# Kernel optimization log

Measured on AMD Instinct MI355X. Metric: run time of the kernel, lower is better.

Reference implementation:

```python
import jax, jax.numpy as jnp
import numpy as np
import math

NUM_EMBED = 1024
EMBED_FEATS = 256
IN_FEATS = 512
COMMITMENT_COST = 0.25
B, T = 16, 4096


def setup_inputs() -> dict:
    key = jax.random.key(0)
    k1, k2, k3, k4 = jax.random.split(key, 4)
    inputs = jax.random.normal(k1, (B, IN_FEATS, T), dtype=jnp.float32)
    # Conv1d(kernel_size=1) == per-position linear: weight [E, C_in], bias [E]
    proj_w = jax.random.normal(k2, (EMBED_FEATS, IN_FEATS), dtype=jnp.float32) / np.sqrt(IN_FEATS)
    proj_b = jax.random.normal(k3, (EMBED_FEATS,), dtype=jnp.float32) * 0.01
    embed = jax.random.normal(k4, (NUM_EMBED, EMBED_FEATS), dtype=jnp.float32)
    return {"inputs": inputs, "proj_w": proj_w, "proj_b": proj_b, "embed": embed}


def reference(inputs, proj_w, proj_b, embed):
    sg = jax.lax.stop_gradient
    b, c_in, t = inputs.shape
    # 1x1 conv projection then transpose(1,-1): [B, T, E]
    x = jnp.einsum('bct,ec->bte', inputs, proj_w) + proj_b
    flat = x.reshape(-1, EMBED_FEATS)  # [B*T, E]
    d2 = (jnp.sum(flat * flat, axis=1, keepdims=True)
          + jnp.sum(embed * embed, axis=1)
          - 2.0 * flat @ embed.T)  # [B*T, num_embed]
    q_idx = jnp.argmin(d2, axis=1)  # [B*T]
    # one-hot @ embed == direct gather (same math, same gradient structure)
    z_q = embed[q_idx].reshape(x.shape)  # [B, T, E]
    vq_loss = jnp.mean((z_q - sg(x)) ** 2)
    commitment_loss = jnp.mean((sg(z_q) - x) ** 2)
    loss = vq_loss + COMMITMENT_COST * commitment_loss
    z_q_st = x + sg(z_q - x)  # straight-through
    n_tokens = flat.shape[0]
    probs = jnp.zeros((NUM_EMBED,), dtype=jnp.float32).at[q_idx].add(1.0) / n_tokens
    log_perplexity = -jnp.sum(probs * jnp.log(probs + 1e-10))
    num_spatial = n_tokens / b
    kldiv_r = math.log(NUM_EMBED) * num_spatial * jnp.ones((b, 1), dtype=jnp.float32)
    z_q_out = jnp.swapaxes(z_q_st, 1, 2)  # [B, E, T]
    return z_q_out, loss, kldiv_r, log_perplexity
```

## Files before the change

### kernel.cpp

```cpp
#include <hip/hip_runtime.h>
#include <hip/hip_bf16.h>
#include <math.h>

#define TT   4096
#define BB   16
#define NTOK 65536
#define CIN  512
#define EF   256
#define NE   1024

typedef __attribute__((ext_vector_type(8))) short bf16x8;
typedef __attribute__((ext_vector_type(4))) float f32x4;

static __device__ __forceinline__ unsigned short f2bf(float f) {
  unsigned int u = __float_as_uint(f);
  u += 0x7fffu + ((u >> 16) & 1u);
  return (unsigned short)(u >> 16);
}

#define GLL(gsrc, ldst) \
  __builtin_amdgcn_global_load_lds((const __attribute__((address_space(1))) void*)(gsrc), \
                                   (__attribute__((address_space(3))) void*)(ldst), 16, 0, 0)

__global__ __launch_bounds__(256) void k_prep(const float* __restrict__ Wf,
                                              const float* __restrict__ Ef,
                                              unsigned short* __restrict__ Wbf,
                                              unsigned short* __restrict__ Ebf,
                                              float* __restrict__ e_norm) {
  int bid = blockIdx.x;
  if (bid < 512) {
    int i = bid * 256 + threadIdx.x;
    Wbf[i] = f2bf(Wf[i]);
  } else if (bid < 1536) {
    int i = (bid - 512) * 256 + threadIdx.x;
    Ebf[i] = f2bf(-2.0f * Ef[i]);
  } else {
    int w = threadIdx.x >> 6, l = threadIdx.x & 63;
    int k = (bid - 1536) * 4 + w;
    const float4 v4 = ((const float4*)(Ef + (size_t)k * EF))[l];
    float s = v4.x * v4.x + v4.y * v4.y + v4.z * v4.z + v4.w * v4.w;
    for (int off = 32; off; off >>= 1) s += __shfl_down(s, off);
    if (l == 0) e_norm[k] = s;
  }
}

__global__ __launch_bounds__(512, 2) void k_fused(const float* __restrict__ in,
                                                  const unsigned short* __restrict__ Wbf,
                                                  const float* __restrict__ bias,
                                                  const unsigned short* __restrict__ Ebf,
                                                  const float* __restrict__ e_norm,
                                                  int* __restrict__ bi_out,
                                                  unsigned int* __restrict__ hist,
                                                  float* __restrict__ sse) {
  __shared__ unsigned short lds[32768];
  unsigned short* as_ = lds;
  unsigned short* bs  = lds + 8192;
  unsigned short* xs  = lds;

  int tid = threadIdx.x;
  int w = tid >> 6, l = tid & 63;
  int l15 = l & 15, quad = l >> 4;
  int tq = w & 1, eq = w >> 1;
  int cg = w & 3, th = w >> 2;
  int tok0 = blockIdx.x * 128;
  const float* src = in + (size_t)(tok0 >> 12) * CIN * TT + (tok0 & 4095);

  f32x4 acc[4][4];
#pragma unroll
  for (int a = 0; a < 4; ++a)
#pragma unroll
    for (int b = 0; b < 4; ++b) acc[a][b] = (f32x4){0.f, 0.f, 0.f, 0.f};

  float v[16];
  {
    const float* s0 = src + (size_t)(cg * 16) * TT + th * 64 + l;
#pragma unroll
    for (int i = 0; i < 16; ++i) v[i] = s0[(size_t)i * TT];
  }
  for (int ks = 0; ks < 8; ++ks) {
    int k0 = ks * 64;
#pragma unroll
    for (int i = 0; i < 4; ++i) {
      int g = i * 512 + tid;
      int row = g >> 3, pc = g & 7, lc = pc ^ (row & 7);
      GLL(Wbf + (size_t)row * CIN + k0 + lc * 8, bs + g * 8);
    }
    int trow = th * 64 + l;
#pragma unroll
    for (int cc = 0; cc < 2; ++cc) {
      alignas(16) unsigned short tmp[8];
#pragma unroll
      for (int j = 0; j < 8; ++j) tmp[j] = f2bf(v[cc * 8 + j]);
      int c8 = cg * 2 + cc;
      int pc = c8 ^ (trow & 7);
      *(bf16x8*)(as_ + trow * 64 + pc * 8) = *(const bf16x8*)tmp;
    }
    __syncthreads();
    if (ks < 7) {
      const float* s0 = src + (size_t)(k0 + 64 + cg * 16) * TT + th * 64 + l;
#pragma unroll
      for (int i = 0; i < 16; ++i) v[i] = s0[(size_t)i * TT];
    }
#pragma unroll
    for (int kstep = 0; kstep < 2; ++kstep) {
      int ck = kstep * 4 + quad;
      bf16x8 af[4], bfr[4];
#pragma unroll
      for (int msub = 0; msub < 4; ++msub) {
        int row = tq * 64 + msub * 16 + l15;
        int pa = ck ^ (row & 7);
        af[msub] = *(const bf16x8*)(as_ + row * 64 + pa * 8);
      }
#pragma unroll
      for (int nsub = 0; nsub < 4; ++nsub) {
        int row = eq * 64 + nsub * 16 + l15;
        int pb = ck ^ (row & 7);
        bfr[nsub] = *(const bf16x8*)(bs + row * 64 + pb * 8);
      }
#pragma unroll
      for (int msub = 0; msub < 4; ++msub)
#pragma unroll
        for (int nsub = 0; nsub < 4; ++nsub)
          acc[msub][nsub] = __builtin_amdgcn_mfma_f32_16x16x32_bf16(af[msub], bfr[nsub],
                                                                    acc[msub][nsub], 0, 0, 0);
    }
    __syncthreads();
  }

  float xsq = 0.f;
#pragma unroll
  for (int nsub = 0; nsub < 4; ++nsub) {
    int e = eq * 64 + nsub * 16 + l15;
    float bv = bias[e];
    int cx = e >> 3;
#pragma unroll
    for (int msub = 0; msub < 4; ++msub)
#pragma unroll
      for (int reg = 0; reg < 4; ++reg) {
        int m = tq * 64 + msub * 16 + quad * 4 + reg;
        float x = acc[msub][nsub][reg] + bv;
        xsq += x * x;
        int pcx = cx ^ (m & 31);
        xs[m * 256 + pcx * 8 + (e & 7)] = f2bf(x);
      }
  }
  __syncthreads();

  int g3 = w & 3, h = w >> 2;
  bf16x8 af[2][8];
#pragma unroll
  for (int msub = 0; msub < 2; ++msub)
#pragma unroll
    for (int kst = 0; kst < 8; ++kst) {
      int row = g3 * 32 + msub * 16 + l15;
      int c32 = kst * 4 + quad;
      int pcx = c32 ^ (row & 31);
      af[msub][kst] = *(const bf16x8*)(xs + row * 256 + pcx * 8);
    }
  __syncthreads();

#pragma unroll
  for (int i = 0; i < 4; ++i) {
    int g = i * 512 + tid;
    int row = g >> 5, pcc = g & 31, lc = pcc ^ (row & 31);
    GLL(Ebf + (size_t)row * EF + lc * 8, lds + g * 8);
  }
  float enn[2];
  enn[0] = e_norm[h * 32 + l15];
  enn[1] = e_norm[h * 32 + 16 + l15];
  __syncthreads();

  float best_v[2][4];
  int best_i[2][4];
#pragma unroll
  for (int a = 0; a < 2; ++a)
#pragma unroll
    for (int b = 0; b < 4; ++b) { best_v[a][b] = 3.0e38f; best_i[a][b] = 0; }

  for (int chunk = 0; chunk < 16; ++chunk) {
    int p = chunk & 1;
    int c0 = chunk * 64;
    unsigned short* eb = lds + p * 16384;
    if (chunk < 15) {
      unsigned short* ebn = lds + (p ^ 1) * 16384;
#pragma unroll
      for (int i = 0; i < 4; ++i) {
        int g = i * 512 + tid;
        int row = g >> 5, pcc = g & 31, lc = pcc ^ (row & 31);
        GLL(Ebf + (size_t)(c0 + 64 + row) * EF + lc * 8, ebn + g * 8);
      }
    }
    f32x4 dacc[2][2];
#pragma unroll
    for (int nsub = 0; nsub < 2; ++nsub) {
      float en = enn[nsub];
#pragma unroll
      for (int msub = 0; msub < 2; ++msub) dacc[msub][nsub] = (f32x4){en, en, en, en};
    }
    if (chunk < 15) {
      enn[0] = e_norm[c0 + 64 + h * 32 + l15];
      enn[1] = e_norm[c0 + 64 + h * 32 + 16 + l15];
    }
#pragma unroll
    for (int nsub = 0; nsub < 2; ++nsub) {
      int r = h * 32 + nsub * 16 + l15;
#pragma unroll
      for (int kst = 0; kst < 8; ++kst) {
        int cc = kst * 4 + quad;
        int pc = cc ^ (r & 31);
        bf16x8 bfr = *(const bf16x8*)(eb + r * 256 + pc * 8);
        dacc[0][nsub] = __builtin_amdgcn_mfma_f32_16x16x32_bf16(af[0][kst], bfr,
                                                                dacc[0][nsub], 0, 0, 0);
        dacc[1][nsub] = __builtin_amdgcn_mfma_f32_16x16x32_bf16(af[1][kst], bfr,
                                                                dacc[1][nsub], 0, 0, 0);
      }
    }
#pragma unroll
    for (int msub = 0; msub < 2; ++msub)
#pragma unroll
      for (int nsub = 0; nsub < 2; ++nsub) {
        int code = c0 + h * 32 + nsub * 16 + l15;
#pragma unroll
        for (int reg = 0; reg < 4; ++reg) {
          float vv = dacc[msub][nsub][reg];
          if (vv < best_v[msub][reg]) { best_v[msub][reg] = vv; best_i[msub][reg] = code; }
        }
      }
    __syncthreads();
  }

#pragma unroll
  for (int msub = 0; msub < 2; ++msub)
#pragma unroll
    for (int reg = 0; reg < 4; ++reg) {
      float vv = best_v[msub][reg];
      int idx = best_i[msub][reg];
#pragma unroll
      for (int off = 8; off; off >>= 1) {
        float ov = __shfl_xor(vv, off, 16);
        int oi = __shfl_xor(idx, off, 16);
        if (ov < vv || (ov == vv && oi < idx)) { vv = ov; idx = oi; }
      }
      best_v[msub][reg] = vv;
      best_i[msub][reg] = idx;
    }
  float* red_v = (float*)lds;
  int* red_i = (int*)lds + 256;
  float* xred = (float*)lds + 512;
  float* svred = (float*)lds + 520;
  if (l15 == 0) {
#pragma unroll
    for (int msub = 0; msub < 2; ++msub)
#pragma unroll
      for (int reg = 0; reg < 4; ++reg) {
        int tokloc = g3 * 32 + msub * 16 + quad * 4 + reg;
        red_v[h * 128 + tokloc] = best_v[msub][reg];
        red_i[h * 128 + tokloc] = best_i[msub][reg];
      }
  }
  for (int off = 32; off; off >>= 1) xsq += __shfl_down(xsq, off);
  if (l == 0) xred[w] = xsq;
  __syncthreads();
  if (tid < 128) {
    float v0 = red_v[tid], v1 = red_v[128 + tid];
    int i0 = red_i[tid], i1 = red_i[128 + tid];
    float vv; int idx;
    if (v1 < v0 || (v1 == v0 && i1 < i0)) { vv = v1; idx = i1; } else { vv = v0; idx = i0; }
    bi_out[tok0 + tid] = idx;
    atomicAdd(&hist[idx], 1u);
    for (int off = 32; off; off >>= 1) vv += __shfl_down(vv, off);
    if ((tid & 63) == 0) svred[tid >> 6] = vv;
  }
  __syncthreads();
  if (tid == 0) {
    float tot = svred[0] + svred[1];
#pragma unroll
    for (int i = 0; i < 8; ++i) tot += xred[i];
    atomicAdd(sse, tot);
  }
}

__global__ __launch_bounds__(256) void k_gather(const float* __restrict__ embed,
                                                const int* __restrict__ bi,
                                                float* __restrict__ out) {
  __shared__ float zq[128 * 65];
  __shared__ int idxs[128];
  int tid = threadIdx.x;
  int tok0 = blockIdx.x * 128;
  int e0 = blockIdx.y * 64;
  if (tid < 128) idxs[tid] = bi[tok0 + tid];
  __syncthreads();
  int l15 = tid & 15, tg = tid >> 4;
  for (int r = 0; r < 8; ++r) {
    int tl = r * 16 + tg;
    const float4 v = *(const float4*)(embed + (size_t)idxs[tl] * EF + e0 + l15 * 4);
    float* zr = zq + tl * 65 + l15 * 4;
    zr[0] = v.x; zr[1] = v.y; zr[2] = v.z; zr[3] = v.w;
  }
  __syncthreads();
  int b = tok0 >> 12, t0 = tok0 & 4095;
  int tl4 = (tid & 31) * 4;
  for (int r = 0; r < 8; ++r) {
    int e = r * 8 + (tid >> 5);
    float4 v;
    v.x = zq[(tl4 + 0) * 65 + e];
    v.y = zq[(tl4 + 1) * 65 + e];
    v.z = zq[(tl4 + 2) * 65 + e];
    v.w = zq[(tl4 + 3) * 65 + e];
    *(float4*)(out + ((size_t)(b * EF + e0 + e) << 12) + t0 + tl4) = v;
  }
}

__global__ __launch_bounds__(256) void k_final(const unsigned int* __restrict__ hist,
                                               const float* __restrict__ sse,
                                               float* __restrict__ out) {
  __shared__ float red[4];
  int tid = threadIdx.x;
  float local = 0.f;
  for (int i = tid; i < NE; i += 256) {
    float p = (float)hist[i] * (1.0f / 65536.0f);
    local -= p * logf(p + 1e-10f);
  }
  for (int off = 32; off; off >>= 1) local += __shfl_down(local, off);
  if ((tid & 63) == 0) red[tid >> 6] = local;
  __syncthreads();
  if (tid == 0) {
    float lp = red[0] + red[1] + red[2] + red[3];
    out[16777216] = 1.25f * sse[0] / 16777216.0f;
    out[16777233] = lp;
  }
  if (tid < 16) out[16777217 + tid] = 6.93147180559945f * 4096.0f;
}

extern "C" void kernel_launch(void* const* d_in, const int* in_sizes, int n_in,
                              void* d_out, int out_size, void* d_ws, size_t ws_size,
                              hipStream_t stream) {
  const float* inputs = (const float*)d_in[0];
  const float* proj_w = (const float*)d_in[1];
  const float* proj_b = (const float*)d_in[2];
  const float* embed = (const float*)d_in[3];
  float* out = (float*)d_out;
  char* ws = (char*)d_ws;

  unsigned short* Wbf  = (unsigned short*)(ws);
  unsigned short* Ebf  = (unsigned short*)(ws + 262144);
  float* e_norm        = (float*)(ws + 786432);
  int* bi              = (int*)(ws + 790528);
  unsigned int* hist   = (unsigned int*)(ws + 1052672);
  float* sse           = (float*)(ws + 1056768);
  if (ws_size < 1056772) return;

  hipMemsetAsync(ws + 1052672, 0, 4100, stream);

  k_prep<<<1792, 256, 0, stream>>>(proj_w, embed, Wbf, Ebf, e_norm);
  k_fused<<<512, 512, 0, stream>>>(inputs, Wbf, proj_b, Ebf, e_norm, bi, hist, sse);
  k_gather<<<dim3(512, 4), 256, 0, stream>>>(embed, bi, out);
  k_final<<<1, 256, 0, stream>>>(hist, sse, out);
}
```

Measured before the change: 292.0 us.

## Fuse codebook gather into main kernel and triple-buffer codebook chunks

Folds the separate gather/transpose kernel into the end of the fused projection+argmin kernel, so indices stay in LDS instead of going through a global buffer and a second launch. The distance loop switches to 32-code chunks in a three-slot LDS ring with partial vmcnt waits and one barrier per chunk. e_norm is staged in LDS, and raw s_waitcnt/s_barrier plus setprio around MFMA blocks replace __syncthreads in the GEMM loop. This adds risk from hand-written wait counts and gives each block a serial tail of gather and store work.

```diff
diff --git a/kernel.cpp b/kernel.cpp
--- a/kernel.cpp
+++ b/kernel.cpp
@@ -49,9 +49,10 @@
                                                   const float* __restrict__ bias,
                                                   const unsigned short* __restrict__ Ebf,
                                                   const float* __restrict__ e_norm,
-                                                  int* __restrict__ bi_out,
+                                                  const float* __restrict__ embed,
                                                   unsigned int* __restrict__ hist,
-                                                  float* __restrict__ sse) {
+                                                  float* __restrict__ sse,
+                                                  float* __restrict__ out) {
   __shared__ unsigned short lds[32768];
   unsigned short* as_ = lds;
   unsigned short* bs  = lds + 8192;
@@ -85,6 +86,7 @@
       int row = g >> 3, pc = g & 7, lc = pc ^ (row & 7);
       GLL(Wbf + (size_t)row * CIN + k0 + lc * 8, bs + g * 8);
     }
+    __builtin_amdgcn_sched_barrier(0);
     int trow = th * 64 + l;
 #pragma unroll
     for (int cc = 0; cc < 2; ++cc) {
@@ -92,14 +94,17 @@
 #pragma unroll
       for (int j = 0; j < 8; ++j) tmp[j] = f2bf(v[cc * 8 + j]);
       int c8 = cg * 2 + cc;
-      int pc = c8 ^ (trow & 7);
-      *(bf16x8*)(as_ + trow * 64 + pc * 8) = *(const bf16x8*)tmp;
-    }
-    __syncthreads();
+      int pc2 = c8 ^ (trow & 7);
+      *(bf16x8*)(as_ + trow * 64 + pc2 * 8) = *(const bf16x8*)tmp;
+    }
     if (ks < 7) {
       const float* s0 = src + (size_t)(k0 + 64 + cg * 16) * TT + th * 64 + l;
 #pragma unroll
       for (int i = 0; i < 16; ++i) v[i] = s0[(size_t)i * TT];
+      __builtin_amdgcn_sched_barrier(0);
+      asm volatile("s_waitcnt vmcnt(16) lgkmcnt(0)\n\ts_barrier" ::: "memory");
+    } else {
+      asm volatile("s_waitcnt vmcnt(0) lgkmcnt(0)\n\ts_barrier" ::: "memory");
     }
 #pragma unroll
     for (int kstep = 0; kstep < 2; ++kstep) {
@@ -117,14 +122,16 @@
         int pb = ck ^ (row & 7);
         bfr[nsub] = *(const bf16x8*)(bs + row * 64 + pb * 8);
       }
+      __builtin_amdgcn_s_setprio(1);
 #pragma unroll
       for (int msub = 0; msub < 4; ++msub)
 #pragma unroll
         for (int nsub = 0; nsub < 4; ++nsub)
           acc[msub][nsub] = __builtin_amdgcn_mfma_f32_16x16x32_bf16(af[msub], bfr[nsub],
                                                                     acc[msub][nsub], 0, 0, 0);
-    }
-    __syncthreads();
+      __builtin_amdgcn_s_setprio(0);
+    }
+    asm volatile("s_waitcnt lgkmcnt(0)\n\ts_barrier" ::: "memory");
   }
 
   float xsq = 0.f;
@@ -159,16 +166,19 @@
     }
   __syncthreads();
 
-#pragma unroll
-  for (int i = 0; i < 4; ++i) {
+  float* entab = (float*)(lds + 24576);
+  {
+    float2 ev = *(const float2*)(e_norm + (tid << 1));
+    *(float2*)(entab + (tid << 1)) = ev;
+  }
+  __builtin_amdgcn_sched_barrier(0);
+#pragma unroll
+  for (int i = 0; i < 2; ++i) {
     int g = i * 512 + tid;
-    int row = g >> 5, pcc = g & 31, lc = pcc ^ (row & 31);
+    int row = g >> 5, pcc = g & 31, lc = pcc ^ row;
     GLL(Ebf + (size_t)row * EF + lc * 8, lds + g * 8);
   }
-  float enn[2];
-  enn[0] = e_norm[h * 32 + l15];
-  enn[1] = e_norm[h * 32 + 16 + l15];
-  __syncthreads();
+  __builtin_amdgcn_sched_barrier(0);
 
   float best_v[2][4];
   int best_i[2][4];
@@ -177,56 +187,49 @@
 #pragma unroll
     for (int b = 0; b < 4; ++b) { best_v[a][b] = 3.0e38f; best_i[a][b] = 0; }
 
-  for (int chunk = 0; chunk < 16; ++chunk) {
-    int p = chunk & 1;
-    int c0 = chunk * 64;
-    unsigned short* eb = lds + p * 16384;
-    if (chunk < 15) {
-      unsigned short* ebn = lds + (p ^ 1) * 16384;
-#pragma unroll
-      for (int i = 0; i < 4; ++i) {
+  int r3 = h * 16 + l15;
+  unsigned short* eb = lds;
+  unsigned short* pf = lds + 8192;
+  int c0 = 0;
+#pragma unroll 1
+  for (int chunk = 0; chunk < 32; ++chunk, c0 += 32) {
+    if (chunk < 31) {
+#pragma unroll
+      for (int i = 0; i < 2; ++i) {
         int g = i * 512 + tid;
-        int row = g >> 5, pcc = g & 31, lc = pcc ^ (row & 31);
-        GLL(Ebf + (size_t)(c0 + 64 + row) * EF + lc * 8, ebn + g * 8);
-      }
-    }
-    f32x4 dacc[2][2];
-#pragma unroll
-    for (int nsub = 0; nsub < 2; ++nsub) {
-      float en = enn[nsub];
-#pragma unroll
-      for (int msub = 0; msub < 2; ++msub) dacc[msub][nsub] = (f32x4){en, en, en, en};
-    }
-    if (chunk < 15) {
-      enn[0] = e_norm[c0 + 64 + h * 32 + l15];
-      enn[1] = e_norm[c0 + 64 + h * 32 + 16 + l15];
-    }
-#pragma unroll
-    for (int nsub = 0; nsub < 2; ++nsub) {
-      int r = h * 32 + nsub * 16 + l15;
-#pragma unroll
-      for (int kst = 0; kst < 8; ++kst) {
-        int cc = kst * 4 + quad;
-        int pc = cc ^ (r & 31);
-        bf16x8 bfr = *(const bf16x8*)(eb + r * 256 + pc * 8);
-        dacc[0][nsub] = __builtin_amdgcn_mfma_f32_16x16x32_bf16(af[0][kst], bfr,
-                                                                dacc[0][nsub], 0, 0, 0);
-        dacc[1][nsub] = __builtin_amdgcn_mfma_f32_16x16x32_bf16(af[1][kst], bfr,
-                                                                dacc[1][nsub], 0, 0, 0);
-      }
-    }
+        int row = g >> 5, pcc = g & 31, lc = pcc ^ row;
+        GLL(Ebf + (size_t)(c0 + 32 + row) * EF + lc * 8, pf + g * 8);
+      }
+      __builtin_amdgcn_sched_barrier(0);
+      asm volatile("s_waitcnt vmcnt(2) lgkmcnt(0)\n\ts_barrier" ::: "memory");
+    } else {
+      asm volatile("s_waitcnt vmcnt(0) lgkmcnt(0)\n\ts_barrier" ::: "memory");
+    }
+    float en = entab[c0 + r3];
+    f32x4 dacc[2];
+    dacc[0] = (f32x4){en, en, en, en};
+    dacc[1] = (f32x4){en, en, en, en};
+    __builtin_amdgcn_s_setprio(1);
+#pragma unroll
+    for (int kst = 0; kst < 8; ++kst) {
+      int cc = kst * 4 + quad;
+      int pc = cc ^ r3;
+      bf16x8 bfr = *(const bf16x8*)(eb + r3 * 256 + pc * 8);
+      dacc[0] = __builtin_amdgcn_mfma_f32_16x16x32_bf16(af[0][kst], bfr, dacc[0], 0, 0, 0);
+      dacc[1] = __builtin_amdgcn_mfma_f32_16x16x32_bf16(af[1][kst], bfr, dacc[1], 0, 0, 0);
+    }
+    __builtin_amdgcn_s_setprio(0);
+    int code = c0 + r3;
 #pragma unroll
     for (int msub = 0; msub < 2; ++msub)
 #pragma unroll
-      for (int nsub = 0; nsub < 2; ++nsub) {
-        int code = c0 + h * 32 + nsub * 16 + l15;
-#pragma unroll
-        for (int reg = 0; reg < 4; ++reg) {
-          float vv = dacc[msub][nsub][reg];
-          if (vv < best_v[msub][reg]) { best_v[msub][reg] = vv; best_i[msub][reg] = code; }
-        }
-      }
-    __syncthreads();
+      for (int reg = 0; reg < 4; ++reg) {
+        float vv = dacc[msub][reg];
+        if (vv < best_v[msub][reg]) { best_v[msub][reg] = vv; best_i[msub][reg] = code; }
+      }
+    eb = pf;
+    pf += 8192;
+    if (pf == lds + 24576) pf = lds;
   }
 
 #pragma unroll
@@ -248,6 +251,7 @@
   int* red_i = (int*)lds + 256;
   float* xred = (float*)lds + 512;
   float* svred = (float*)lds + 520;
+  int* fidx_w = (int*)lds + 544;
   if (l15 == 0) {
 #pragma unroll
     for (int msub = 0; msub < 2; ++msub)
@@ -266,7 +270,7 @@
     int i0 = red_i[tid], i1 = red_i[128 + tid];
     float vv; int idx;
     if (v1 < v0 || (v1 == v0 && i1 < i0)) { vv = v1; idx = i1; } else { vv = v0; idx = i0; }
-    bi_out[tok0 + tid] = idx;
+    fidx_w[tid] = idx;
     atomicAdd(&hist[idx], 1u);
     for (int off = 32; off; off >>= 1) vv += __shfl_down(vv, off);
     if ((tid & 63) == 0) svred[tid >> 6] = vv;
@@ -278,36 +282,34 @@
     for (int i = 0; i < 8; ++i) tot += xred[i];
     atomicAdd(sse, tot);
   }
-}
-
-__global__ __launch_bounds__(256) void k_gather(const float* __restrict__ embed,
-                                                const int* __restrict__ bi,
-                                                float* __restrict__ out) {
-  __shared__ float zq[128 * 65];
-  __shared__ int idxs[128];
-  int tid = threadIdx.x;
-  int tok0 = blockIdx.x * 128;
-  int e0 = blockIdx.y * 64;
-  if (tid < 128) idxs[tid] = bi[tok0 + tid];
-  __syncthreads();
-  int l15 = tid & 15, tg = tid >> 4;
-  for (int r = 0; r < 8; ++r) {
-    int tl = r * 16 + tg;
-    const float4 v = *(const float4*)(embed + (size_t)idxs[tl] * EF + e0 + l15 * 4);
-    float* zr = zq + tl * 65 + l15 * 4;
-    zr[0] = v.x; zr[1] = v.y; zr[2] = v.z; zr[3] = v.w;
-  }
-  __syncthreads();
-  int b = tok0 >> 12, t0 = tok0 & 4095;
-  int tl4 = (tid & 31) * 4;
-  for (int r = 0; r < 8; ++r) {
-    int e = r * 8 + (tid >> 5);
-    float4 v;
-    v.x = zq[(tl4 + 0) * 65 + e];
-    v.y = zq[(tl4 + 1) * 65 + e];
-    v.z = zq[(tl4 + 2) * 65 + e];
-    v.w = zq[(tl4 + 3) * 65 + e];
-    *(float4*)(out + ((size_t)(b * EF + e0 + e) << 12) + t0 + tl4) = v;
+
+  const int* fidx = (const int*)lds + 544;
+  float* zq = (float*)lds + 1024;
+  int bnum = tok0 >> 12, t0 = tok0 & 4095;
+  float* outb = out + (((size_t)bnum * EF) << 12) + t0;
+#pragma unroll 1
+  for (int et = 0; et < 4; ++et) {
+    int e0 = et * 64;
+#pragma unroll
+    for (int rr = 0; rr < 4; ++rr) {
+      int tl = rr * 32 + (tid >> 4);
+      const float4 g4 = *(const float4*)(embed + (size_t)fidx[tl] * EF + e0 + (tid & 15) * 4);
+      float* zr = zq + tl * 65 + (tid & 15) * 4;
+      zr[0] = g4.x; zr[1] = g4.y; zr[2] = g4.z; zr[3] = g4.w;
+    }
+    __syncthreads();
+#pragma unroll
+    for (int rr = 0; rr < 4; ++rr) {
+      int e = rr * 16 + (tid >> 5);
+      int tc = (tid & 31) * 4;
+      float4 o4;
+      o4.x = zq[(tc + 0) * 65 + e];
+      o4.y = zq[(tc + 1) * 65 + e];
+      o4.z = zq[(tc + 2) * 65 + e];
+      o4.w = zq[(tc + 3) * 65 + e];
+      *(float4*)(outb + ((size_t)(e0 + e) << 12) + tc) = o4;
+    }
+    if (et < 3) __syncthreads();
   }
 }
 
@@ -345,7 +347,6 @@
   unsigned short* Wbf  = (unsigned short*)(ws);
   unsigned short* Ebf  = (unsigned short*)(ws + 262144);
   float* e_norm        = (float*)(ws + 786432);
-  int* bi              = (int*)(ws + 790528);
   unsigned int* hist   = (unsigned int*)(ws + 1052672);
   float* sse           = (float*)(ws + 1056768);
   if (ws_size < 1056772) return;
@@ -353,7 +354,6 @@
   hipMemsetAsync(ws + 1052672, 0, 4100, stream);
 
   k_prep<<<1792, 256, 0, stream>>>(proj_w, embed, Wbf, Ebf, e_norm);
-  k_fused<<<512, 512, 0, stream>>>(inputs, Wbf, proj_b, Ebf, e_norm, bi, hist, sse);
-  k_gather<<<dim3(512, 4), 256, 0, stream>>>(embed, bi, out);
+  k_fused<<<512, 512, 0, stream>>>(inputs, Wbf, proj_b, Ebf, e_norm, embed, hist, sse, out);
   k_final<<<1, 256, 0, stream>>>(hist, sse, out);
 }
```

New measurement: 293.1 us. No clear change (+0.4%).
